# Optimization experiments

Hardware: AMD Instinct MI355X
Metric: run time of the kernel (lower is better)

## Reference

```python
import jax, jax.numpy as jnp
import numpy as np

LRELU_SLOPE = 0.2
SQRT2 = 1.4142135623730951

def make_coord(h, w):
    # LIIF make_coord: cell-center coords in [-1, 1]; index 0 is the row (dim -2) coord.
    ys = -1.0 + (2.0 * jnp.arange(h, dtype=jnp.float32) + 1.0) / h
    xs = -1.0 + (2.0 * jnp.arange(w, dtype=jnp.float32) + 1.0) / w
    yy, xx = jnp.meshgrid(ys, xs, indexing='ij')
    return jnp.stack([yy, xx], axis=-1).reshape(h * w, 2)  # [Q, 2]

def style_layer(x, style_vec, scale2, shift, mod_w, mod_b, conv_w, act_b):
    # StyleGAN2-style modulated 3x3 conv + instance norm + (scale2, shift) affine + fused leaky relu.
    s = style_vec @ mod_w.T + mod_b                                   # [B, Cin] modulation
    w = conv_w[None] * s[:, None, :, None, None]                      # [B, Cout, Cin, 3, 3]
    demod = jax.lax.rsqrt(jnp.sum(w * w, axis=(2, 3, 4)) + 1e-8)      # [B, Cout]
    y = jax.lax.conv_general_dilated(x * s[:, :, None, None], conv_w, (1, 1), 'SAME',
                                     dimension_numbers=('NCHW', 'OIHW', 'NCHW'))
    y = y * demod[:, :, None, None]
    mu = jnp.mean(y, axis=(2, 3), keepdims=True)
    var = jnp.var(y, axis=(2, 3), keepdims=True)
    y = (y - mu) * jax.lax.rsqrt(var + 1e-5)                          # InstanceNorm2d (no affine)
    y = y * scale2 + shift
    return jax.nn.leaky_relu(y + act_b[None, :, None, None], LRELU_SLOPE) * SQRT2

def reference(x, scale1, scale2, shift, mod_w, mod_b, conv_w, act_b, w1, b1, w2, b2, out_h, out_w):
    B, C, Hf, Wf = x.shape
    feat = style_layer(x, scale1, scale2, shift, mod_w, mod_b, conv_w, act_b)
    Q = out_h * out_w
    coord = jnp.broadcast_to(make_coord(out_h, out_w)[None], (B, Q, 2))  # [B, Q, 2]
    rx = 1.0 / Hf  # = 2/Hf/2
    ry = 1.0 / Wf
    eps_shift = 1e-6
    feat_flat = feat.reshape(B, C, Hf * Wf).transpose(0, 2, 1)  # [B, Hf*Wf, C]
    preds, areas = [], []
    for vx in (-1, 1):
        for vy in (-1, 1):
            cy = jnp.clip(coord[..., 0] + vx * rx + eps_shift, -1.0 + 1e-6, 1.0 - 1e-6)
            cx = jnp.clip(coord[..., 1] + vy * ry + eps_shift, -1.0 + 1e-6, 1.0 - 1e-6)
            # nearest grid_sample (align_corners=False): idx = floor((c+1)/2 * size)
            iy = jnp.clip(jnp.floor((cy + 1.0) * 0.5 * Hf), 0, Hf - 1).astype(jnp.int32)
            ix = jnp.clip(jnp.floor((cx + 1.0) * 0.5 * Wf), 0, Wf - 1).astype(jnp.int32)
            lin = iy * Wf + ix                                        # [B, Q]
            q_feat = jnp.take_along_axis(feat_flat, lin[..., None], axis=1)  # [B, Q, C]
            qy = -1.0 + (2.0 * iy.astype(jnp.float32) + 1.0) / Hf     # nearest feat-cell coord
            qx = -1.0 + (2.0 * ix.astype(jnp.float32) + 1.0) / Wf
            rel_y = (coord[..., 0] - qy) * Hf
            rel_x = (coord[..., 1] - qx) * Wf
            inp = jnp.concatenate([q_feat, rel_y[..., None], rel_x[..., None]], axis=-1)  # [B,Q,C+2]
            pred = (inp @ w1 + b1) @ w2 + b2                          # two stacked Linears, no act
            preds.append(pred)
            areas.append(jnp.abs(rel_y * rel_x) + 1e-9)
    tot_area = areas[0] + areas[1] + areas[2] + areas[3]
    areas = [areas[3], areas[2], areas[1], areas[0]]  # diagonal swap (local ensemble)
    ret = jnp.zeros_like(preds[0])
    for pred, area in zip(preds, areas):
        ret = ret + pred * (area / tot_area)[..., None]
    return ret  # [B, Q, dim]

def setup_inputs() -> dict:
    key = jax.random.key(0)
    ks = jax.random.split(key, 12)
    B, C, Hf, Wf, S = 4, 64, 64, 64, 512
    return {
        'x': jax.random.normal(ks[0], (B, C, Hf, Wf), jnp.float32),
        'scale1': jax.random.normal(ks[1], (B, S), jnp.float32),
        'scale2': jax.random.normal(ks[2], (B, C, 1, 1), jnp.float32),
        'shift': jax.random.normal(ks[3], (B, C, 1, 1), jnp.float32),
        'mod_w': jax.random.normal(ks[4], (C, S), jnp.float32) * 0.02,
        'mod_b': jnp.ones((C,), jnp.float32),
        'conv_w': jax.random.normal(ks[5], (C, C, 3, 3), jnp.float32) * 0.05,
        'act_b': jax.random.normal(ks[6], (C,), jnp.float32) * 0.02,
        'w1': jax.random.normal(ks[7], (C + 2, 256), jnp.float32) * 0.05,
        'b1': jax.random.normal(ks[8], (256,), jnp.float32) * 0.01,
        'w2': jax.random.normal(ks[9], (256, C), jnp.float32) * 0.05,
        'b2': jax.random.normal(ks[10], (C,), jnp.float32) * 0.01,
        'out_h': 256,
        'out_w': 256,
    }
```

## Files before the change

### kernel.cpp

```cpp
#include <hip/hip_runtime.h>

#define SQRT2F 1.41421356237309515f

typedef __attribute__((ext_vector_type(8))) short bf16x8;
typedef __attribute__((ext_vector_type(4))) float f32x4;

enum : int {
  DM_OFF   = 0,
  BC_OFF   = 256,
  WC_OFF   = 1024,
  P_OFF    = 8192,
  Y_OFF    = 65536,
  WS_FLOATS = Y_OFF + 1048576
};

__device__ __align__(16) float WS[WS_FLOATS];
__device__ __align__(256) unsigned bar_cnt[4 * 64];
__device__ __align__(256) unsigned bar_gen[4 * 64];

__device__ __forceinline__ unsigned ld_llcu(const unsigned* p) {
  unsigned v;
  asm volatile("global_load_dword %0, %1, off sc0 sc1\n\ts_waitcnt vmcnt(0)"
               : "=v"(v) : "v"(p) : "memory");
  return v;
}
__device__ __forceinline__ float ld_llcf(const float* p) {
  float v;
  asm volatile("global_load_dword %0, %1, off sc0 sc1\n\ts_waitcnt vmcnt(0)"
               : "=v"(v) : "v"(p) : "memory");
  return v;
}
__device__ __forceinline__ f32x4 ld_llc4(const float* p) {
  f32x4 v;
  asm volatile("global_load_dwordx4 %0, %1, off sc0 sc1\n\ts_waitcnt vmcnt(0)"
               : "=v"(v) : "v"(p) : "memory");
  return v;
}
__device__ __forceinline__ void stg_llc1(float* p, float v) {
  asm volatile("global_store_dword %0, %1, off sc0 sc1"
               :: "v"(p), "v"(v) : "memory");
}
__device__ __forceinline__ void stg_llc4(float* p, f32x4 v) {
  asm volatile("global_store_dwordx4 %0, %1, off sc0 sc1"
               :: "v"(p), "v"(v) : "memory");
}

struct ConvSh {
  unsigned short Xl[3 * 66 * 64];
  unsigned short Wl[64 * 24 * 8];
  float part[512];
  float s_sh[64];
};
struct GoutSh {
  float ft[100][68];
  float G[100][68];
  float red[2048];
  float A[64], B[64];
};
union ShU { ConvSh c; GoutSh g; };

__device__ __forceinline__ unsigned short f2bf(float v) {
  unsigned int u = __float_as_uint(v);
  u += 0x7fffu + ((u >> 16) & 1u);
  return (unsigned short)(u >> 16);
}

__global__ __launch_bounds__(512) void mega_kernel(
    const float* __restrict__ x,      const float* __restrict__ scale1,
    const float* __restrict__ scale2, const float* __restrict__ shiftp,
    const float* __restrict__ mod_w,  const float* __restrict__ mod_b,
    const float* __restrict__ conv_w, const float* __restrict__ act_b,
    const float* __restrict__ b1,     const float* __restrict__ w2,
    const float* __restrict__ b2,     const float* __restrict__ w1,
    float* __restrict__ out) {
  const int bid = blockIdx.x;
  const int b = bid >> 6;
  const int r = bid & 63;
  const int t = threadIdx.x;
  const int w = t >> 6, lane = t & 63;
  const int l15 = lane & 15, l4 = lane >> 4;

  __shared__ __align__(16) ShU sh;

  {
    const int i = t >> 3, qq = t & 7;
    const float* sv = scale1 + b * 512 + qq * 64;
    const float* mw = mod_w + i * 512 + qq * 64;
    float p = 0.f;
    for (int k = 0; k < 64; ++k) p += sv[k] * mw[k];
    sh.c.part[t] = p;
  }
  __syncthreads();
  if ((t & 7) == 0) {
    const int i = t >> 3;
    float s = mod_b[i];
    #pragma unroll
    for (int k = 0; k < 8; ++k) s += sh.c.part[t + k];
    sh.c.s_sh[i] = s;
  }
  __syncthreads();

  if (r == 0) {
    const int o = t >> 3, qq = t & 7;
    const float* cw = conv_w + o * 576 + qq * 72;
    float d = 0.f;
    #pragma unroll
    for (int ii = 0; ii < 8; ++ii) {
      const float ss = sh.c.s_sh[qq * 8 + ii];
      float wsq = 0.f;
      #pragma unroll
      for (int k = 0; k < 9; ++k) { const float wv = cw[ii * 9 + k]; wsq += wv * wv; }
      d += ss * ss * wsq;
    }
    sh.c.part[t] = d;
    __syncthreads();
    if ((t & 7) == 0) {
      float dd = 1e-8f;
      #pragma unroll
      for (int k = 0; k < 8; ++k) dd += sh.c.part[t + k];
      stg_llc1(&WS[DM_OFF + b * 64 + (t >> 3)], rsqrtf(dd));
    }
    __syncthreads();
  }

  if (r >= 1 && r <= 8) {
    const int idx = (r - 1) * 512 + t;
    const int c = idx >> 6, o = idx & 63;
    const float* r1 = w1 + c * 256;
    float a = 0.f;
    for (int k = 0; k < 256; ++k) a = fmaf(r1[k], w2[k * 64 + o], a);
    stg_llc1(&WS[WC_OFF + idx], a);
  } else if (r == 9) {
    if (t < 128) {
      const int idx = 4096 + t;
      const int c = idx >> 6, o = idx & 63;
      const float* r1 = w1 + c * 256;
      float a = 0.f;
      for (int k = 0; k < 256; ++k) a = fmaf(r1[k], w2[k * 64 + o], a);
      stg_llc1(&WS[WC_OFF + idx], a);
    } else if (t < 192) {
      const int o = t - 128;
      float a = 0.f;
      for (int k = 0; k < 256; ++k) a = fmaf(b1[k], w2[k * 64 + o], a);
      stg_llc1(&WS[BC_OFF + o], a + b2[o]);
    }
  }

  {
    int4* Xz = (int4*)sh.c.Xl;
    int4 z; z.x = z.y = z.z = z.w = 0;
    for (int idx = t; idx < 1584; idx += 512) Xz[idx] = z;
  }
  __syncthreads();

  {
    const int col = t & 63;
    const int tq = t >> 6;
    unsigned int* Xw = (unsigned int*)sh.c.Xl;
    for (int it = 0; it < 12; ++it) {
      const int task = it * 8 + tq;
      const int row3 = task >> 5;
      const int ich = (task & 31) * 2;
      const int rr = r - 1 + row3;
      if (rr >= 0 && rr < 64) {
        const float* xb = x + ((size_t)(b * 64 + ich) << 12) + (rr << 6) + col;
        const float v0 = xb[0] * sh.c.s_sh[ich];
        const float v1 = xb[4096] * sh.c.s_sh[ich + 1];
        const unsigned int u = (unsigned int)f2bf(v0) | ((unsigned int)f2bf(v1) << 16);
        const int colp = col + 1;
        const int byte = ((row3 * 66 + colp) << 7) + ((((ich >> 3)) ^ (colp & 7)) << 4) + ((ich & 7) << 1);
        Xw[byte >> 2] = u;
      }
    }
  }

  const int oh = w >> 2, pg = w & 3;
  f32x4 acc[2];
  acc[0] = (f32x4){0.f, 0.f, 0.f, 0.f};
  acc[1] = (f32x4){0.f, 0.f, 0.f, 0.f};

  const bf16x8* Xv = (const bf16x8*)sh.c.Xl;
  const bf16x8* Wv = (const bf16x8*)sh.c.Wl;
  int4* Wst = (int4*)sh.c.Wl;

  for (int dy = 0; dy < 3; ++dy) {
    __syncthreads();
    #pragma unroll
    for (int i = 0; i < 3; ++i) {
      const int idx = i * 512 + t;
      const int o = idx / 24;
      const int g = idx - o * 24;
      const int dx = g >> 3, gg = g & 7;
      const float* cw = conv_w + o * 576 + (gg * 8) * 9 + dy * 3 + dx;
      int4 v;
      v.x = (int)((unsigned int)f2bf(cw[0])  | ((unsigned int)f2bf(cw[9])  << 16));
      v.y = (int)((unsigned int)f2bf(cw[18]) | ((unsigned int)f2bf(cw[27]) << 16));
      v.z = (int)((unsigned int)f2bf(cw[36]) | ((unsigned int)f2bf(cw[45]) << 16));
      v.w = (int)((unsigned int)f2bf(cw[54]) | ((unsigned int)f2bf(cw[63]) << 16));
      Wst[o * 24 + dx * 8 + (gg ^ (o & 7))] = v;
    }
    __syncthreads();

    #pragma unroll
    for (int dx = 0; dx < 3; ++dx) {
      #pragma unroll
      for (int kh = 0; kh < 2; ++kh) {
        const int kg = kh * 4 + l4;
        bf16x8 afr[2];
        #pragma unroll
        for (int m = 0; m < 2; ++m) {
          const int o = oh * 32 + m * 16 + l15;
          afr[m] = Wv[o * 24 + dx * 8 + (kg ^ (o & 7))];
        }
        const int colp = pg * 16 + l15 + dx;
        const bf16x8 bfr = Xv[((dy * 66 + colp) << 3) + (kg ^ (colp & 7))];
        #pragma unroll
        for (int m = 0; m < 2; ++m)
          acc[m] = __builtin_amdgcn_mfma_f32_16x16x32_bf16(
              afr[m], bfr, acc[m], 0, 0, 0);
      }
    }
  }

  {
    const int px = pg * 16 + l15;
    float* yq = WS + Y_OFF + (((size_t)b * 4096 + r * 64 + px) << 6);
    #pragma unroll
    for (int m = 0; m < 2; ++m)
      stg_llc4(yq + oh * 32 + m * 16 + l4 * 4, acc[m]);
  }

  __syncthreads();
  {
    float* sred = sh.c.part;
    #pragma unroll
    for (int m = 0; m < 2; ++m) {
      #pragma unroll
      for (int j = 0; j < 4; ++j) {
        float s1 = acc[m][j];
        float s2 = acc[m][j] * acc[m][j];
        #pragma unroll
        for (int off = 1; off < 16; off <<= 1) {
          s1 += __shfl_xor(s1, off);
          s2 += __shfl_xor(s2, off);
        }
        if (l15 == 0) {
          const int ol = m * 16 + l4 * 4 + j;
          sred[(w * 32 + ol) * 2 + 0] = s1;
          sred[(w * 32 + ol) * 2 + 1] = s2;
        }
      }
    }
    __syncthreads();
    if (t < 128) {
      const int o = t >> 1, wh = t & 1;
      const int ohh = o >> 5, ol = o & 31;
      float s = 0.f;
      #pragma unroll
      for (int pq = 0; pq < 4; ++pq)
        s += sred[(((ohh * 4 + pq) * 32) + ol) * 2 + wh];
      stg_llc1(&WS[P_OFF + (((size_t)b * 64 + r) * 64 + o) * 2 + wh], s);
    }
  }

  asm volatile("s_waitcnt vmcnt(0)" ::: "memory");
  __syncthreads();
  if (t == 0) {
    unsigned* cnt = &bar_cnt[b * 64];
    unsigned* gen = &bar_gen[b * 64];
    const unsigned g0 = ld_llcu(gen);
    const unsigned old = __hip_atomic_fetch_add(cnt, 1u, __ATOMIC_RELAXED,
                                                __HIP_MEMORY_SCOPE_AGENT);
    if (old == 63u) {
      __hip_atomic_store(cnt, 0u, __ATOMIC_RELAXED, __HIP_MEMORY_SCOPE_AGENT);
      __hip_atomic_fetch_add(gen, 1u, __ATOMIC_RELAXED,
                             __HIP_MEMORY_SCOPE_AGENT);
    } else {
      while (ld_llcu(gen) == g0) __builtin_amdgcn_s_sleep(8);
    }
  }
  __syncthreads();

  const int ty = (bid >> 3) & 7;
  const int tx = bid & 7;
  float* WcL = &sh.g.G[0][0];

  {
    f32x4 ps = (f32x4){0.f, 0.f, 0.f, 0.f};
    const float* Pb = WS + P_OFF + (size_t)b * 8192;
    #pragma unroll
    for (int k = 0; k < 4; ++k) {
      const f32x4 v = ld_llc4(Pb + (size_t)(t + k * 512) * 4);
      ps += v;
    }
    *(f32x4*)&sh.g.red[(t >> 5) * 128 + (t & 31) * 4] = ps;

    for (int i4 = t; i4 < 1072; i4 += 512) {
      const f32x4 v = (i4 < 1056) ? ld_llc4(WS + WC_OFF + i4 * 4)
                                  : ld_llc4(WS + BC_OFF + (i4 - 1056) * 4);
      *(f32x4*)&WcL[i4 * 4] = v;
    }
  }
  __syncthreads();

  float wcreg[64];
  #pragma unroll
  for (int c = 0; c < 64; ++c) wcreg[c] = WcL[c * 64 + lane];
  const float bcv = WcL[4224 + lane];
  const int sub = t & 3, chb = sub * 16;
  float4 wa[4], wb[4];
  #pragma unroll
  for (int k = 0; k < 4; ++k) {
    wa[k] = *(const float4*)&WcL[64 * 64 + chb + k * 4];
    wb[k] = *(const float4*)&WcL[65 * 64 + chb + k * 4];
  }
  if (t < 64) {
    float S1 = 0.f, S2 = 0.f;
    #pragma unroll
    for (int m = 0; m < 16; ++m) {
      S1 += sh.g.red[m * 128 + t * 2];
      S2 += sh.g.red[m * 128 + t * 2 + 1];
    }
    const float mu = S1 * (1.f / 4096.f);
    const float var = S2 * (1.f / 4096.f) - mu * mu;
    const float dm = ld_llcf(WS + DM_OFF + b * 64 + t);
    const float rstd = rsqrtf(dm * dm * var + 1e-5f);
    const float A = dm * rstd * scale2[b * 64 + t];
    sh.g.A[t] = A;
    sh.g.B[t] = -mu * A + shiftp[b * 64 + t] + act_b[t];
  }
  __syncthreads();

  const int cy_base = ty * 8 - 1, cx_base = tx * 8 - 1;
  {
    const float4* A4 = (const float4*)sh.g.A;
    const float4* B4 = (const float4*)sh.g.B;
    const float* yb = WS + Y_OFF + ((size_t)b << 18);
    for (int f = t; f < 1600; f += 512) {
      const int cell = f >> 4, cq = f & 15;
      const int li = cell / 10, lj = cell - li * 10;
      const int ciy = cy_base + li, cix = cx_base + lj;
      if (ciy >= 0 && ciy < 64 && cix >= 0 && cix < 64) {
        const f32x4 y4 = ld_llc4(yb + (((size_t)(ciy << 6) + cix) << 6) + cq * 4);
        const float4 Av = A4[cq], Bv = B4[cq];
        float4 fv;
        float u;
        u = y4[0] * Av.x + Bv.x; fv.x = (u > 0.f ? u : 0.2f * u) * SQRT2F;
        u = y4[1] * Av.y + Bv.y; fv.y = (u > 0.f ? u : 0.2f * u) * SQRT2F;
        u = y4[2] * Av.z + Bv.z; fv.z = (u > 0.f ? u : 0.2f * u) * SQRT2F;
        u = y4[3] * Av.w + Bv.w; fv.w = (u > 0.f ? u : 0.2f * u) * SQRT2F;
        *(float4*)&sh.g.ft[cell][cq * 4] = fv;
      }
    }
  }
  __syncthreads();

  {
    #pragma unroll
    for (int p = 0; p < 4; ++p) {
      const int cb = p * 32 + w * 4;
      if (cb < 100) {
        #pragma unroll
        for (int i2 = 0; i2 < 4; ++i2) {
          float a = bcv;
          const float* fr = sh.g.ft[cb + i2];
          #pragma unroll
          for (int c = 0; c < 64; c += 4) {
            const float4 fv = *(const float4*)&fr[c];
            a = fmaf(fv.x, wcreg[c], a);
            a = fmaf(fv.y, wcreg[c + 1], a);
            a = fmaf(fv.z, wcreg[c + 2], a);
            a = fmaf(fv.w, wcreg[c + 3], a);
          }
          sh.g.G[cb + i2][lane] = a;
        }
      }
    }
  }
  __syncthreads();

  const float lo = -1.f + 1e-6f, hi = 1.f - 1e-6f;
  #pragma unroll 1
  for (int pass = 0; pass < 8; ++pass) {
    const int qi = pass * 128 + (t >> 2);
    const int oy = (ty << 5) + (qi >> 5), ox = (tx << 5) + (qi & 31);

    const float cy0 = -1.f + (2.f * oy + 1.f) * (1.f / 256.f);
    const float cx0 = -1.f + (2.f * ox + 1.f) * (1.f / 256.f);

    int lcell[4];
    float area[4], rely[4], relx[4];
    int j = 0;
    #pragma unroll
    for (int vx = -1; vx <= 1; vx += 2) {
      #pragma unroll
      for (int vy = -1; vy <= 1; vy += 2) {
        float cy = cy0 + (float)vx * (1.f / 64.f) + 1e-6f;
        cy = fminf(fmaxf(cy, lo), hi);
        float cx = cx0 + (float)vy * (1.f / 64.f) + 1e-6f;
        cx = fminf(fmaxf(cx, lo), hi);
        const float fy = floorf((cy + 1.f) * 32.f);
        const float fx = floorf((cx + 1.f) * 32.f);
        const int iy = (int)fminf(fmaxf(fy, 0.f), 63.f);
        const int ix = (int)fminf(fmaxf(fx, 0.f), 63.f);
        const float qy = -1.f + (2.f * iy + 1.f) * (1.f / 64.f);
        const float qx = -1.f + (2.f * ix + 1.f) * (1.f / 64.f);
        const float ry_ = (cy0 - qy) * 64.f;
        const float rx_ = (cx0 - qx) * 64.f;
        lcell[j] = (iy - cy_base) * 10 + (ix - cx_base);
        rely[j] = ry_; relx[j] = rx_;
        area[j] = fabsf(ry_ * rx_) + 1e-9f;
        ++j;
      }
    }
    const float tot = area[0] + area[1] + area[2] + area[3];
    float wgt[4];
    #pragma unroll
    for (int k = 0; k < 4; ++k) wgt[k] = area[3 - k] / tot;
    const float swy = wgt[0] * rely[0] + wgt[1] * rely[1] + wgt[2] * rely[2] + wgt[3] * rely[3];
    const float swx = wgt[0] * relx[0] + wgt[1] * relx[1] + wgt[2] * relx[2] + wgt[3] * relx[3];

    float4 rr[4];
    #pragma unroll
    for (int k = 0; k < 4; ++k) {
      rr[k].x = swy * wa[k].x + swx * wb[k].x;
      rr[k].y = swy * wa[k].y + swx * wb[k].y;
      rr[k].z = swy * wa[k].z + swx * wb[k].z;
      rr[k].w = swy * wa[k].w + swx * wb[k].w;
    }
    #pragma unroll
    for (int jj = 0; jj < 4; ++jj) {
      const float4* gp = (const float4*)&sh.g.G[lcell[jj]][chb];
      const float wv = wgt[jj];
      #pragma unroll
      for (int k = 0; k < 4; ++k) {
        const float4 gv = gp[k];
        rr[k].x += wv * gv.x; rr[k].y += wv * gv.y;
        rr[k].z += wv * gv.z; rr[k].w += wv * gv.w;
      }
    }
    const size_t gq = ((size_t)b << 16) + (oy << 8) + ox;
    float4* op = (float4*)(out + (gq << 6) + chb);
    #pragma unroll
    for (int k = 0; k < 4; ++k) op[k] = rr[k];
  }
}

extern "C" void kernel_launch(void* const* d_in, const int* in_sizes, int n_in,
                              void* d_out, int out_size, void* d_ws, size_t ws_size,
                              hipStream_t stream) {
  (void)in_sizes; (void)n_in; (void)out_size; (void)d_ws; (void)ws_size;
  const float* x      = (const float*)d_in[0];
  const float* scale1 = (const float*)d_in[1];
  const float* scale2 = (const float*)d_in[2];
  const float* shiftp = (const float*)d_in[3];
  const float* mod_w  = (const float*)d_in[4];
  const float* mod_b  = (const float*)d_in[5];
  const float* conv_w = (const float*)d_in[6];
  const float* act_b  = (const float*)d_in[7];
  const float* w1     = (const float*)d_in[8];
  const float* b1     = (const float*)d_in[9];
  const float* w2     = (const float*)d_in[10];
  const float* b2     = (const float*)d_in[11];
  float* out = (float*)d_out;

  hipLaunchKernelGGL(mega_kernel, dim3(256), dim3(512), 0, stream,
                     x, scale1, scale2, shiftp, mod_w, mod_b, conv_w, act_b,
                     b1, w2, b2, w1, out);
}
```

Before: 68.83 us.

## Double grid to 512 blocks, split conv and weight-fold work onto separate blocks

Launches 128 blocks per batch instead of 64. The first 64 blocks per batch do the conv rows, block 64 computes demodulation, and blocks 65-73 fold w1·w2 and the bias, so these prologue tasks no longer run serially inside the conv blocks. The output phase tiles change to 16x32 pixels per block, with smaller shared ft/G buffers. Fewer pixels per block and more resident blocks should raise occupancy on the many CUs, but the grid-wide barrier now has to wait for twice as many blocks and the feature halo overlap grows.

```diff
diff --git a/kernel.cpp b/kernel.cpp
--- a/kernel.cpp
+++ b/kernel.cpp
@@ -52,8 +52,8 @@
   float s_sh[64];
 };
 struct GoutSh {
-  float ft[100][68];
-  float G[100][68];
+  float ft[60][68];
+  float G[64][68];
   float red[2048];
   float A[64], B[64];
 };
@@ -74,33 +74,35 @@
     const float* __restrict__ b2,     const float* __restrict__ w1,
     float* __restrict__ out) {
   const int bid = blockIdx.x;
-  const int b = bid >> 6;
-  const int r = bid & 63;
+  const int b = bid >> 7;
+  const int pb = bid & 127;
   const int t = threadIdx.x;
   const int w = t >> 6, lane = t & 63;
   const int l15 = lane & 15, l4 = lane >> 4;
 
   __shared__ __align__(16) ShU sh;
 
-  {
-    const int i = t >> 3, qq = t & 7;
-    const float* sv = scale1 + b * 512 + qq * 64;
-    const float* mw = mod_w + i * 512 + qq * 64;
-    float p = 0.f;
-    for (int k = 0; k < 64; ++k) p += sv[k] * mw[k];
-    sh.c.part[t] = p;
-  }
-  __syncthreads();
-  if ((t & 7) == 0) {
-    const int i = t >> 3;
-    float s = mod_b[i];
-    #pragma unroll
-    for (int k = 0; k < 8; ++k) s += sh.c.part[t + k];
-    sh.c.s_sh[i] = s;
-  }
-  __syncthreads();
-
-  if (r == 0) {
+  if (pb <= 64) {
+    {
+      const int i = t >> 3, qq = t & 7;
+      const float* sv = scale1 + b * 512 + qq * 64;
+      const float* mw = mod_w + i * 512 + qq * 64;
+      float p = 0.f;
+      for (int k = 0; k < 64; ++k) p = fmaf(sv[k], mw[k], p);
+      sh.c.part[t] = p;
+    }
+    __syncthreads();
+    if ((t & 7) == 0) {
+      const int i = t >> 3;
+      float s = mod_b[i];
+      #pragma unroll
+      for (int k = 0; k < 8; ++k) s += sh.c.part[t + k];
+      sh.c.s_sh[i] = s;
+    }
+    __syncthreads();
+  }
+
+  if (pb == 64) {
     const int o = t >> 3, qq = t & 7;
     const float* cw = conv_w + o * 576 + qq * 72;
     float d = 0.f;
@@ -120,146 +122,140 @@
       for (int k = 0; k < 8; ++k) dd += sh.c.part[t + k];
       stg_llc1(&WS[DM_OFF + b * 64 + (t >> 3)], rsqrtf(dd));
     }
-    __syncthreads();
-  }
-
-  if (r >= 1 && r <= 8) {
-    const int idx = (r - 1) * 512 + t;
-    const int c = idx >> 6, o = idx & 63;
-    const float* r1 = w1 + c * 256;
-    float a = 0.f;
-    for (int k = 0; k < 256; ++k) a = fmaf(r1[k], w2[k * 64 + o], a);
-    stg_llc1(&WS[WC_OFF + idx], a);
-  } else if (r == 9) {
-    if (t < 128) {
-      const int idx = 4096 + t;
+  } else if (pb >= 65 && pb < 74) {
+    const int idx = (pb - 65) * 512 + t;
+    if (idx < 4224) {
       const int c = idx >> 6, o = idx & 63;
       const float* r1 = w1 + c * 256;
       float a = 0.f;
       for (int k = 0; k < 256; ++k) a = fmaf(r1[k], w2[k * 64 + o], a);
       stg_llc1(&WS[WC_OFF + idx], a);
-    } else if (t < 192) {
-      const int o = t - 128;
+    } else if (idx < 4288) {
+      const int o = idx - 4224;
       float a = 0.f;
       for (int k = 0; k < 256; ++k) a = fmaf(b1[k], w2[k * 64 + o], a);
       stg_llc1(&WS[BC_OFF + o], a + b2[o]);
     }
   }
 
-  {
-    int4* Xz = (int4*)sh.c.Xl;
-    int4 z; z.x = z.y = z.z = z.w = 0;
-    for (int idx = t; idx < 1584; idx += 512) Xz[idx] = z;
-  }
-  __syncthreads();
-
-  {
-    const int col = t & 63;
-    const int tq = t >> 6;
-    unsigned int* Xw = (unsigned int*)sh.c.Xl;
-    for (int it = 0; it < 12; ++it) {
-      const int task = it * 8 + tq;
-      const int row3 = task >> 5;
-      const int ich = (task & 31) * 2;
-      const int rr = r - 1 + row3;
-      if (rr >= 0 && rr < 64) {
-        const float* xb = x + ((size_t)(b * 64 + ich) << 12) + (rr << 6) + col;
-        const float v0 = xb[0] * sh.c.s_sh[ich];
-        const float v1 = xb[4096] * sh.c.s_sh[ich + 1];
-        const unsigned int u = (unsigned int)f2bf(v0) | ((unsigned int)f2bf(v1) << 16);
-        const int colp = col + 1;
-        const int byte = ((row3 * 66 + colp) << 7) + ((((ich >> 3)) ^ (colp & 7)) << 4) + ((ich & 7) << 1);
-        Xw[byte >> 2] = u;
-      }
-    }
-  }
-
-  const int oh = w >> 2, pg = w & 3;
-  f32x4 acc[2];
-  acc[0] = (f32x4){0.f, 0.f, 0.f, 0.f};
-  acc[1] = (f32x4){0.f, 0.f, 0.f, 0.f};
-
-  const bf16x8* Xv = (const bf16x8*)sh.c.Xl;
-  const bf16x8* Wv = (const bf16x8*)sh.c.Wl;
-  int4* Wst = (int4*)sh.c.Wl;
-
-  for (int dy = 0; dy < 3; ++dy) {
+  if (pb < 64) {
+    const int r = pb;
+    {
+      int4* Xz = (int4*)sh.c.Xl;
+      int4 z; z.x = z.y = z.z = z.w = 0;
+      for (int idx = t; idx < 1584; idx += 512) Xz[idx] = z;
+    }
     __syncthreads();
-    #pragma unroll
-    for (int i = 0; i < 3; ++i) {
-      const int idx = i * 512 + t;
-      const int o = idx / 24;
-      const int g = idx - o * 24;
-      const int dx = g >> 3, gg = g & 7;
-      const float* cw = conv_w + o * 576 + (gg * 8) * 9 + dy * 3 + dx;
-      int4 v;
-      v.x = (int)((unsigned int)f2bf(cw[0])  | ((unsigned int)f2bf(cw[9])  << 16));
-      v.y = (int)((unsigned int)f2bf(cw[18]) | ((unsigned int)f2bf(cw[27]) << 16));
-      v.z = (int)((unsigned int)f2bf(cw[36]) | ((unsigned int)f2bf(cw[45]) << 16));
-      v.w = (int)((unsigned int)f2bf(cw[54]) | ((unsigned int)f2bf(cw[63]) << 16));
-      Wst[o * 24 + dx * 8 + (gg ^ (o & 7))] = v;
-    }
+
+    {
+      const int col = t & 63;
+      const int tq = t >> 6;
+      unsigned int* Xw = (unsigned int*)sh.c.Xl;
+      #pragma unroll
+      for (int it = 0; it < 12; ++it) {
+        const int task = it * 8 + tq;
+        const int row3 = task >> 5;
+        const int ich = (task & 31) * 2;
+        const int rr = r - 1 + row3;
+        if (rr >= 0 && rr < 64) {
+          const float* xb = x + ((size_t)(b * 64 + ich) << 12) + (rr << 6) + col;
+          const float v0 = xb[0] * sh.c.s_sh[ich];
+          const float v1 = xb[4096] * sh.c.s_sh[ich + 1];
+          const unsigned int u = (unsigned int)f2bf(v0) | ((unsigned int)f2bf(v1) << 16);
+          const int colp = col + 1;
+          const int byte = ((row3 * 66 + colp) << 7) + ((((ich >> 3)) ^ (colp & 7)) << 4) + ((ich & 7) << 1);
+          Xw[byte >> 2] = u;
+        }
+      }
+    }
+
+    const int oh = w >> 2, pg = w & 3;
+    f32x4 acc[2];
+    acc[0] = (f32x4){0.f, 0.f, 0.f, 0.f};
+    acc[1] = (f32x4){0.f, 0.f, 0.f, 0.f};
+
+    const bf16x8* Xv = (const bf16x8*)sh.c.Xl;
+    const bf16x8* Wv = (const bf16x8*)sh.c.Wl;
+    int4* Wst = (int4*)sh.c.Wl;
+
+    for (int dy = 0; dy < 3; ++dy) {
+      __syncthreads();
+      #pragma unroll
+      for (int i = 0; i < 3; ++i) {
+        const int idx = i * 512 + t;
+        const int o = idx / 24;
+        const int g = idx - o * 24;
+        const int dx = g >> 3, gg = g & 7;
+        const float* cw = conv_w + o * 576 + (gg * 8) * 9 + dy * 3 + dx;
+        int4 v;
+        v.x = (int)((unsigned int)f2bf(cw[0])  | ((unsigned int)f2bf(cw[9])  << 16));
+        v.y = (int)((unsigned int)f2bf(cw[18]) | ((unsigned int)f2bf(cw[27]) << 16));
+        v.z = (int)((unsigned int)f2bf(cw[36]) | ((unsigned int)f2bf(cw[45]) << 16));
+        v.w = (int)((unsigned int)f2bf(cw[54]) | ((unsigned int)f2bf(cw[63]) << 16));
+        Wst[o * 24 + dx * 8 + (gg ^ (o & 7))] = v;
+      }
+      __syncthreads();
+
+      #pragma unroll
+      for (int dx = 0; dx < 3; ++dx) {
+        #pragma unroll
+        for (int kh = 0; kh < 2; ++kh) {
+          const int kg = kh * 4 + l4;
+          bf16x8 afr[2];
+          #pragma unroll
+          for (int m = 0; m < 2; ++m) {
+            const int o = oh * 32 + m * 16 + l15;
+            afr[m] = Wv[o * 24 + dx * 8 + (kg ^ (o & 7))];
+          }
+          const int colp = pg * 16 + l15 + dx;
+          const bf16x8 bfr = Xv[((dy * 66 + colp) << 3) + (kg ^ (colp & 7))];
+          #pragma unroll
+          for (int m = 0; m < 2; ++m)
+            acc[m] = __builtin_amdgcn_mfma_f32_16x16x32_bf16(
+                afr[m], bfr, acc[m], 0, 0, 0);
+        }
+      }
+    }
+
+    {
+      const int px = pg * 16 + l15;
+      float* yq = WS + Y_OFF + (((size_t)b * 4096 + r * 64 + px) << 6);
+      #pragma unroll
+      for (int m = 0; m < 2; ++m)
+        stg_llc4(yq + oh * 32 + m * 16 + l4 * 4, acc[m]);
+    }
+
     __syncthreads();
-
-    #pragma unroll
-    for (int dx = 0; dx < 3; ++dx) {
-      #pragma unroll
-      for (int kh = 0; kh < 2; ++kh) {
-        const int kg = kh * 4 + l4;
-        bf16x8 afr[2];
+    {
+      float* sred = sh.c.part;
+      #pragma unroll
+      for (int m = 0; m < 2; ++m) {
         #pragma unroll
-        for (int m = 0; m < 2; ++m) {
-          const int o = oh * 32 + m * 16 + l15;
-          afr[m] = Wv[o * 24 + dx * 8 + (kg ^ (o & 7))];
+        for (int j = 0; j < 4; ++j) {
+          float s1 = acc[m][j];
+          float s2 = acc[m][j] * acc[m][j];
+          #pragma unroll
+          for (int off = 1; off < 16; off <<= 1) {
+            s1 += __shfl_xor(s1, off);
+            s2 += __shfl_xor(s2, off);
+          }
+          if (l15 == 0) {
+            const int ol = m * 16 + l4 * 4 + j;
+            sred[(w * 32 + ol) * 2 + 0] = s1;
+            sred[(w * 32 + ol) * 2 + 1] = s2;
+          }
         }
-        const int colp = pg * 16 + l15 + dx;
-        const bf16x8 bfr = Xv[((dy * 66 + colp) << 3) + (kg ^ (colp & 7))];
+      }
+      __syncthreads();
+      if (t < 128) {
+        const int o = t >> 1, wh = t & 1;
+        const int ohh = o >> 5, ol = o & 31;
+        float s = 0.f;
         #pragma unroll
-        for (int m = 0; m < 2; ++m)
-          acc[m] = __builtin_amdgcn_mfma_f32_16x16x32_bf16(
-              afr[m], bfr, acc[m], 0, 0, 0);
-      }
-    }
-  }
-
-  {
-    const int px = pg * 16 + l15;
-    float* yq = WS + Y_OFF + (((size_t)b * 4096 + r * 64 + px) << 6);
-    #pragma unroll
-    for (int m = 0; m < 2; ++m)
-      stg_llc4(yq + oh * 32 + m * 16 + l4 * 4, acc[m]);
-  }
-
-  __syncthreads();
-  {
-    float* sred = sh.c.part;
-    #pragma unroll
-    for (int m = 0; m < 2; ++m) {
-      #pragma unroll
-      for (int j = 0; j < 4; ++j) {
-        float s1 = acc[m][j];
-        float s2 = acc[m][j] * acc[m][j];
-        #pragma unroll
-        for (int off = 1; off < 16; off <<= 1) {
-          s1 += __shfl_xor(s1, off);
-          s2 += __shfl_xor(s2, off);
-        }
-        if (l15 == 0) {
-          const int ol = m * 16 + l4 * 4 + j;
-          sred[(w * 32 + ol) * 2 + 0] = s1;
-          sred[(w * 32 + ol) * 2 + 1] = s2;
-        }
-      }
-    }
-    __syncthreads();
-    if (t < 128) {
-      const int o = t >> 1, wh = t & 1;
-      const int ohh = o >> 5, ol = o & 31;
-      float s = 0.f;
-      #pragma unroll
-      for (int pq = 0; pq < 4; ++pq)
-        s += sred[(((ohh * 4 + pq) * 32) + ol) * 2 + wh];
-      stg_llc1(&WS[P_OFF + (((size_t)b * 64 + r) * 64 + o) * 2 + wh], s);
+        for (int pq = 0; pq < 4; ++pq)
+          s += sred[(((ohh * 4 + pq) * 32) + ol) * 2 + wh];
+        stg_llc1(&WS[P_OFF + (((size_t)b * 64 + r) * 64 + o) * 2 + wh], s);
+      }
     }
   }
 
@@ -271,7 +267,7 @@
     const unsigned g0 = ld_llcu(gen);
     const unsigned old = __hip_atomic_fetch_add(cnt, 1u, __ATOMIC_RELAXED,
                                                 __HIP_MEMORY_SCOPE_AGENT);
-    if (old == 63u) {
+    if (old == 127u) {
       __hip_atomic_store(cnt, 0u, __ATOMIC_RELAXED, __HIP_MEMORY_SCOPE_AGENT);
       __hip_atomic_fetch_add(gen, 1u, __ATOMIC_RELAXED,
                              __HIP_MEMORY_SCOPE_AGENT);
@@ -281,8 +277,8 @@
   }
   __syncthreads();
 
-  const int ty = (bid >> 3) & 7;
-  const int tx = bid & 7;
+  const int ty = pb >> 3;
+  const int tx = pb & 7;
   float* WcL = &sh.g.G[0][0];
 
   {
@@ -331,12 +327,12 @@
   }
   __syncthreads();
 
-  const int cy_base = ty * 8 - 1, cx_base = tx * 8 - 1;
+  const int cy_base = ty * 4 - 1, cx_base = tx * 8 - 1;
   {
     const float4* A4 = (const float4*)sh.g.A;
     const float4* B4 = (const float4*)sh.g.B;
     const float* yb = WS + Y_OFF + ((size_t)b << 18);
-    for (int f = t; f < 1600; f += 512) {
+    for (int f = t; f < 960; f += 512) {
       const int cell = f >> 4, cq = f & 15;
       const int li = cell / 10, lj = cell - li * 10;
       const int ciy = cy_base + li, cix = cx_base + lj;
@@ -357,9 +353,9 @@
 
   {
     #pragma unroll
-    for (int p = 0; p < 4; ++p) {
+    for (int p = 0; p < 2; ++p) {
       const int cb = p * 32 + w * 4;
-      if (cb < 100) {
+      if (cb < 60) {
         #pragma unroll
         for (int i2 = 0; i2 < 4; ++i2) {
           float a = bcv;
@@ -381,9 +377,9 @@
 
   const float lo = -1.f + 1e-6f, hi = 1.f - 1e-6f;
   #pragma unroll 1
-  for (int pass = 0; pass < 8; ++pass) {
+  for (int pass = 0; pass < 4; ++pass) {
     const int qi = pass * 128 + (t >> 2);
-    const int oy = (ty << 5) + (qi >> 5), ox = (tx << 5) + (qi & 31);
+    const int oy = (ty << 4) + (qi >> 5), ox = (tx << 5) + (qi & 31);
 
     const float cy0 = -1.f + (2.f * oy + 1.f) * (1.f / 256.f);
     const float cx0 = -1.f + (2.f * ox + 1.f) * (1.f / 256.f);
@@ -464,7 +460,7 @@
   const float* b2     = (const float*)d_in[11];
   float* out = (float*)d_out;
 
-  hipLaunchKernelGGL(mega_kernel, dim3(256), dim3(512), 0, stream,
+  hipLaunchKernelGGL(mega_kernel, dim3(512), dim3(512), 0, stream,
                      x, scale1, scale2, shiftp, mod_w, mod_b, conv_w, act_b,
                      b1, w2, b2, w1, out);
 }
```

New measurement: 74.53 us. +8.3%, slower.
